# Kernel tuning notes

Hardware: AMD Instinct MI355X
Metric: run time of the kernel (lower is better)

The kernel has to match this reference:

```python
import jax, jax.numpy as jnp
from jax import lax
import numpy as np

WIN_SIZE = 11
WIN_SIGMA = 1.5
K1, K2 = 0.01, 0.03
DATA_RANGE = 1.0


def _gauss_win(size=WIN_SIZE, sigma=WIN_SIGMA):
    coords = np.arange(size, dtype=np.float32) - size // 2
    g = np.exp(-(coords ** 2) / (2.0 * sigma ** 2))
    g /= g.sum()
    return jnp.asarray(g, dtype=jnp.float32)


def _gaussian_blur(x, win):
    # separable depthwise Gaussian blur, VALID padding (as in pytorch-msssim)
    C = x.shape[1]
    dn = ('NCHW', 'OIHW', 'NCHW')
    kh = jnp.tile(win.reshape(1, 1, -1, 1), (C, 1, 1, 1))  # (C,1,K,1)
    kw = jnp.tile(win.reshape(1, 1, 1, -1), (C, 1, 1, 1))  # (C,1,1,K)
    x = lax.conv_general_dilated(x, kh, (1, 1), 'VALID',
                                 dimension_numbers=dn, feature_group_count=C)
    x = lax.conv_general_dilated(x, kw, (1, 1), 'VALID',
                                 dimension_numbers=dn, feature_group_count=C)
    return x


def _ssim_loss(x, y):
    # normalize (-1,1) -> (0,1)
    x = (x + 1.0) * 0.5
    y = (y + 1.0) * 0.5

    c1 = (K1 * DATA_RANGE) ** 2
    c2 = (K2 * DATA_RANGE) ** 2
    win = _gauss_win().astype(x.dtype)

    mu1 = _gaussian_blur(x, win)
    mu2 = _gaussian_blur(y, win)
    mu1_sq = mu1 * mu1
    mu2_sq = mu2 * mu2
    mu1_mu2 = mu1 * mu2

    sigma1_sq = _gaussian_blur(x * x, win) - mu1_sq
    sigma2_sq = _gaussian_blur(y * y, win) - mu2_sq
    sigma12 = _gaussian_blur(x * y, win) - mu1_mu2

    cs_map = (2.0 * sigma12 + c2) / (sigma1_sq + sigma2_sq + c2)
    ssim_map = ((2.0 * mu1_mu2 + c1) / (mu1_sq + mu2_sq + c1)) * cs_map

    # per-channel spatial mean -> nonnegative -> global mean (size_average=True)
    ssim_per_channel = jnp.mean(ssim_map, axis=(2, 3))  # (B, C)
    ssim_per_channel = jax.nn.relu(ssim_per_channel)    # nonnegative_ssim
    return 1.0 - jnp.mean(ssim_per_channel)


def setup_inputs() -> dict:
    key = jax.random.key(0)
    k1, k2 = jax.random.split(key)
    shape = (32, 3, 512, 512)
    return {
        'input': jax.random.normal(k1, shape, dtype=jnp.float32),
        'target': jax.random.normal(k2, shape, dtype=jnp.float32),
    }


def reference(input, target):
    return _ssim_loss(input, target)
```

## Files before the change

### kernel.cpp

```cpp
#include <hip/hip_runtime.h>
#include <math.h>

typedef float f32x2 __attribute__((ext_vector_type(2)));

#define NCH 96
#define HH 512
#define WW 512
#define OH 502
#define STRIP 32
#define NSTRIP 16
#define NT 256

struct Win { float w[11]; };

__device__ __forceinline__ f32x2 pkfma(f32x2 a, f32x2 b, f32x2 c) {
    return __builtin_elementwise_fma(a, b, c);
}

__device__ __forceinline__ float ssim_px(float m1, float m2, float ms, float mp) {
    const float C1v = 1e-4f;
    const float C2v = 9e-4f;
    float mu12  = m1 * m2;
    float musum = fmaf(m1, m1, m2 * m2);
    float num = fmaf(2.f, mp - mu12, C2v) * fmaf(2.f, mu12, C1v);
    float den = ((ms - musum) + C2v) * (musum + C1v);
    return num * __builtin_amdgcn_rcpf(den);
}

#define HB(T0,T1,T2,T3,T4,T5,T6,T7,T8,T9,T10) \
  pkfma(T10, Wv[10], pkfma(T9, Wv[9], pkfma(T8, Wv[8], pkfma(T7, Wv[7], \
  pkfma(T6, Wv[6], pkfma(T5, Wv[5], pkfma(T4, Wv[4], pkfma(T3, Wv[3], \
  pkfma(T2, Wv[2], pkfma(T1, Wv[1], T0 * Wv[0]))))))))))

__global__ __launch_bounds__(NT, 4)
void ssim_main(const float* __restrict__ X, const float* __restrict__ Y,
               float* __restrict__ partial, Win win) {
    __shared__ float4 Eb[2][256];
    __shared__ float4 Ob[2][256];
    __shared__ float red[4];

    const int b     = blockIdx.x;
    const int ch    = b >> 4;
    const int strip = b & 15;
    const int r0    = strip * STRIP;
    const int rows  = min(STRIP, OH - r0);
    const int t     = threadIdx.x;

    f32x2 Wv[11];
    #pragma unroll
    for (int i = 0; i < 11; ++i) Wv[i] = (f32x2){win.w[i], win.w[i]};
    const f32x2 h2 = {0.5f, 0.5f};

    const size_t choff = (size_t)ch * (HH * WW);
    const float* xcol = X + choff + 2 * t;
    const float* ycol = Y + choff + 2 * t;

    f32x2 xs[10], ys[10];

    #pragma unroll
    for (int i = 0; i < 10; ++i) {
        f32x2 xv = *(const f32x2*)(xcol + (size_t)(r0 + i) * WW);
        f32x2 yv = *(const f32x2*)(ycol + (size_t)(r0 + i) * WW);
        xs[i] = pkfma(xv, h2, h2);
        ys[i] = pkfma(yv, h2, h2);
    }
    f32x2 hx = *(const f32x2*)(xcol + (size_t)(r0 + 10) * WW);
    f32x2 hy = *(const f32x2*)(ycol + (size_t)(r0 + 10) * WW);

    float acc = 0.f;

    for (int r = 0; r < rows; ++r) {
        const int buf = r & 1;
        f32x2 nx = pkfma(hx, h2, h2);
        f32x2 ny = pkfma(hy, h2, h2);
        f32x2 ns = pkfma(ny, ny, nx * nx);
        f32x2 np = nx * ny;

        f32x2 vx = nx * Wv[10], vy = ny * Wv[10];
        f32x2 vs = ns * Wv[10], vp = np * Wv[10];
        #pragma unroll
        for (int k = 0; k < 10; ++k) {
            f32x2 xk = xs[k], yk = ys[k];
            f32x2 sk = pkfma(yk, yk, xk * xk);
            f32x2 pk = xk * yk;
            vx = pkfma(xk, Wv[k], vx);
            vy = pkfma(yk, Wv[k], vy);
            vs = pkfma(sk, Wv[k], vs);
            vp = pkfma(pk, Wv[k], vp);
        }
        Eb[buf][t] = make_float4(vx.x, vy.x, vs.x, vp.x);
        Ob[buf][t] = make_float4(vx.y, vy.y, vs.y, vp.y);

        #pragma unroll
        for (int k = 0; k < 9; ++k) { xs[k] = xs[k + 1]; ys[k] = ys[k + 1]; }
        xs[9] = nx; ys[9] = ny;

        {
            const int g = min(r0 + r + 11, HH - 1);
            hx = *(const f32x2*)(xcol + (size_t)g * WW);
            hy = *(const f32x2*)(ycol + (size_t)g * WW);
        }

        __syncthreads();
        if (t <= 250) {
            const float4* Ep = Eb[buf];
            const float4* Op = Ob[buf];
            float4 e0 = Ep[t],     e1 = Ep[t + 1], e2 = Ep[t + 2];
            float4 e3 = Ep[t + 3], e4 = Ep[t + 4], e5 = Ep[t + 5];
            float4 o0 = Op[t],     o1 = Op[t + 1], o2 = Op[t + 2];
            float4 o3 = Op[t + 3], o4 = Op[t + 4], o5 = Op[t + 5];
            f32x2 e0m = {e0.x, e0.y}, e1m = {e1.x, e1.y}, e2m = {e2.x, e2.y};
            f32x2 e3m = {e3.x, e3.y}, e4m = {e4.x, e4.y}, e5m = {e5.x, e5.y};
            f32x2 o0m = {o0.x, o0.y}, o1m = {o1.x, o1.y}, o2m = {o2.x, o2.y};
            f32x2 o3m = {o3.x, o3.y}, o4m = {o4.x, o4.y}, o5m = {o5.x, o5.y};
            f32x2 e0s = {e0.z, e0.w}, e1s = {e1.z, e1.w}, e2s = {e2.z, e2.w};
            f32x2 e3s = {e3.z, e3.w}, e4s = {e4.z, e4.w}, e5s = {e5.z, e5.w};
            f32x2 o0s = {o0.z, o0.w}, o1s = {o1.z, o1.w}, o2s = {o2.z, o2.w};
            f32x2 o3s = {o3.z, o3.w}, o4s = {o4.z, o4.w}, o5s = {o5.z, o5.w};

            f32x2 Am = HB(e0m,o0m,e1m,o1m,e2m,o2m,e3m,o3m,e4m,o4m,e5m);
            f32x2 As = HB(e0s,o0s,e1s,o1s,e2s,o2s,e3s,o3s,e4s,o4s,e5s);
            f32x2 Bm = HB(o0m,e1m,o1m,e2m,o2m,e3m,o3m,e4m,o4m,e5m,o5m);
            f32x2 Bs = HB(o0s,e1s,o1s,e2s,o2s,e3s,o3s,e4s,o4s,e5s,o5s);

            acc += ssim_px(Am.x, Am.y, As.x, As.y);
            acc += ssim_px(Bm.x, Bm.y, Bs.x, Bs.y);
        }
    }

    #pragma unroll
    for (int m = 1; m < 64; m <<= 1) acc += __shfl_xor(acc, m, 64);
    __syncthreads();
    if ((t & 63) == 0) red[t >> 6] = acc;
    __syncthreads();
    if (t == 0) partial[b] = (red[0] + red[1]) + (red[2] + red[3]);
}

__global__ __launch_bounds__(128)
void ssim_final(const float* __restrict__ partial, float* __restrict__ out) {
    const int t = threadIdx.x;
    float v = 0.f;
    if (t < NCH) {
        float s = 0.f;
        #pragma unroll
        for (int i = 0; i < NSTRIP; ++i) s += partial[t * NSTRIP + i];
        s *= (1.f / (502.f * 502.f));
        v = fmaxf(s, 0.f);
    }
    #pragma unroll
    for (int m = 1; m < 64; m <<= 1) v += __shfl_xor(v, m, 64);
    __shared__ float r2[2];
    if ((t & 63) == 0) r2[t >> 6] = v;
    __syncthreads();
    if (t == 0) out[0] = 1.f - (r2[0] + r2[1]) * (1.f / (float)NCH);
}

extern "C" void kernel_launch(void* const* d_in, const int* in_sizes, int n_in,
                              void* d_out, int out_size, void* d_ws, size_t ws_size,
                              hipStream_t stream) {
    const float* X = (const float*)d_in[0];
    const float* Y = (const float*)d_in[1];
    float* out = (float*)d_out;
    float* partial = (float*)d_ws;

    Win win;
    double g[11], sum = 0.0;
    for (int i = 0; i < 11; ++i) {
        double c = (double)(i - 5);
        g[i] = exp(-(c * c) / (2.0 * 1.5 * 1.5));
        sum += g[i];
    }
    for (int i = 0; i < 11; ++i) win.w[i] = (float)(g[i] / sum);

    ssim_main<<<NCH * NSTRIP, NT, 0, stream>>>(X, Y, partial, win);
    ssim_final<<<1, 128, 0, stream>>>(partial, out);
}
```

Before: 86.80 us.

## Compute two output rows per iteration to share vertical-blur work and halve barriers

```diff
diff --git a/kernel.cpp b/kernel.cpp
--- a/kernel.cpp
+++ b/kernel.cpp
@@ -15,6 +15,14 @@
 
 __device__ __forceinline__ f32x2 pkfma(f32x2 a, f32x2 b, f32x2 c) {
     return __builtin_elementwise_fma(a, b, c);
+}
+__device__ __forceinline__ f32x2 pkfmas(f32x2 a, float s, f32x2 c) {
+    f32x2 sv = {s, s};
+    return __builtin_elementwise_fma(a, sv, c);
+}
+__device__ __forceinline__ f32x2 pkmuls(f32x2 a, float s) {
+    f32x2 sv = {s, s};
+    return a * sv;
 }
 
 __device__ __forceinline__ float ssim_px(float m1, float m2, float ms, float mp) {
@@ -28,15 +36,15 @@
 }
 
 #define HB(T0,T1,T2,T3,T4,T5,T6,T7,T8,T9,T10) \
-  pkfma(T10, Wv[10], pkfma(T9, Wv[9], pkfma(T8, Wv[8], pkfma(T7, Wv[7], \
-  pkfma(T6, Wv[6], pkfma(T5, Wv[5], pkfma(T4, Wv[4], pkfma(T3, Wv[3], \
-  pkfma(T2, Wv[2], pkfma(T1, Wv[1], T0 * Wv[0]))))))))))
+  pkfmas(T10, w10, pkfmas(T9, w9, pkfmas(T8, w8, pkfmas(T7, w7, \
+  pkfmas(T6, w6, pkfmas(T5, w5, pkfmas(T4, w4, pkfmas(T3, w3, \
+  pkfmas(T2, w2, pkfmas(T1, w1, pkmuls(T0, w0)))))))))))
 
 __global__ __launch_bounds__(NT, 4)
 void ssim_main(const float* __restrict__ X, const float* __restrict__ Y,
                float* __restrict__ partial, Win win) {
-    __shared__ float4 Eb[2][256];
-    __shared__ float4 Ob[2][256];
+    __shared__ float4 Mb[2][2][256];
+    __shared__ float4 Sb[2][2][256];
     __shared__ float red[4];
 
     const int b     = blockIdx.x;
@@ -46,9 +54,9 @@
     const int rows  = min(STRIP, OH - r0);
     const int t     = threadIdx.x;
 
-    f32x2 Wv[11];
-    #pragma unroll
-    for (int i = 0; i < 11; ++i) Wv[i] = (f32x2){win.w[i], win.w[i]};
+    const float w0 = win.w[0], w1 = win.w[1], w2 = win.w[2], w3 = win.w[3];
+    const float w4 = win.w[4], w5 = win.w[5], w6 = win.w[6], w7 = win.w[7];
+    const float w8 = win.w[8], w9 = win.w[9], w10 = win.w[10];
     const f32x2 h2 = {0.5f, 0.5f};
 
     const size_t choff = (size_t)ch * (HH * WW);
@@ -56,7 +64,6 @@
     const float* ycol = Y + choff + 2 * t;
 
     f32x2 xs[10], ys[10];
-
     #pragma unroll
     for (int i = 0; i < 10; ++i) {
         f32x2 xv = *(const f32x2*)(xcol + (size_t)(r0 + i) * WW);
@@ -64,67 +71,88 @@
         xs[i] = pkfma(xv, h2, h2);
         ys[i] = pkfma(yv, h2, h2);
     }
-    f32x2 hx = *(const f32x2*)(xcol + (size_t)(r0 + 10) * WW);
-    f32x2 hy = *(const f32x2*)(ycol + (size_t)(r0 + 10) * WW);
+    f32x2 hx1 = *(const f32x2*)(xcol + (size_t)(r0 + 10) * WW);
+    f32x2 hy1 = *(const f32x2*)(ycol + (size_t)(r0 + 10) * WW);
+    f32x2 hx2 = *(const f32x2*)(xcol + (size_t)(r0 + 11) * WW);
+    f32x2 hy2 = *(const f32x2*)(ycol + (size_t)(r0 + 11) * WW);
 
     float acc = 0.f;
 
-    for (int r = 0; r < rows; ++r) {
-        const int buf = r & 1;
-        f32x2 nx = pkfma(hx, h2, h2);
-        f32x2 ny = pkfma(hy, h2, h2);
-        f32x2 ns = pkfma(ny, ny, nx * nx);
-        f32x2 np = nx * ny;
-
-        f32x2 vx = nx * Wv[10], vy = ny * Wv[10];
-        f32x2 vs = ns * Wv[10], vp = np * Wv[10];
+    for (int r = 0; r < rows; r += 2) {
+        const int set = (r >> 1) & 1;
+        f32x2 n1x = pkfma(hx1, h2, h2), n1y = pkfma(hy1, h2, h2);
+        f32x2 n2x = pkfma(hx2, h2, h2), n2y = pkfma(hy2, h2, h2);
+        f32x2 n1s = pkfma(n1y, n1y, n1x * n1x), n1p = n1x * n1y;
+        f32x2 n2s = pkfma(n2y, n2y, n2x * n2x), n2p = n2x * n2y;
+
+        f32x2 uAx = pkmuls(n1x, w10), uAy = pkmuls(n1y, w10);
+        f32x2 uAs = pkmuls(n1s, w10), uAp = pkmuls(n1p, w10);
+        f32x2 uBx = pkfmas(n1x, w9, pkmuls(n2x, w10));
+        f32x2 uBy = pkfmas(n1y, w9, pkmuls(n2y, w10));
+        f32x2 uBs = pkfmas(n1s, w9, pkmuls(n2s, w10));
+        f32x2 uBp = pkfmas(n1p, w9, pkmuls(n2p, w10));
         #pragma unroll
         for (int k = 0; k < 10; ++k) {
-            f32x2 xk = xs[k], yk = ys[k];
-            f32x2 sk = pkfma(yk, yk, xk * xk);
-            f32x2 pk = xk * yk;
-            vx = pkfma(xk, Wv[k], vx);
-            vy = pkfma(yk, Wv[k], vy);
-            vs = pkfma(sk, Wv[k], vs);
-            vp = pkfma(pk, Wv[k], vp);
+            const float wk = win.w[k];
+            f32x2 qx = xs[k], qy = ys[k];
+            f32x2 qs = pkfma(qy, qy, qx * qx), qp = qx * qy;
+            uAx = pkfmas(qx, wk, uAx); uAy = pkfmas(qy, wk, uAy);
+            uAs = pkfmas(qs, wk, uAs); uAp = pkfmas(qp, wk, uAp);
+            if (k >= 1) {
+                const float wk1 = win.w[k - 1];
+                uBx = pkfmas(qx, wk1, uBx); uBy = pkfmas(qy, wk1, uBy);
+                uBs = pkfmas(qs, wk1, uBs); uBp = pkfmas(qp, wk1, uBp);
+            }
         }
-        Eb[buf][t] = make_float4(vx.x, vy.x, vs.x, vp.x);
-        Ob[buf][t] = make_float4(vx.y, vy.y, vs.y, vp.y);
+        Mb[set][0][t] = make_float4(uAx.x, uAy.x, uAx.y, uAy.y);
+        Sb[set][0][t] = make_float4(uAs.x, uAp.x, uAs.y, uAp.y);
+        Mb[set][1][t] = make_float4(uBx.x, uBy.x, uBx.y, uBy.y);
+        Sb[set][1][t] = make_float4(uBs.x, uBp.x, uBs.y, uBp.y);
 
         #pragma unroll
-        for (int k = 0; k < 9; ++k) { xs[k] = xs[k + 1]; ys[k] = ys[k + 1]; }
-        xs[9] = nx; ys[9] = ny;
+        for (int k = 0; k < 8; ++k) { xs[k] = xs[k + 2]; ys[k] = ys[k + 2]; }
+        xs[8] = n1x; ys[8] = n1y; xs[9] = n2x; ys[9] = n2y;
 
         {
-            const int g = min(r0 + r + 11, HH - 1);
-            hx = *(const f32x2*)(xcol + (size_t)g * WW);
-            hy = *(const f32x2*)(ycol + (size_t)g * WW);
+            const int g1 = min(r0 + r + 12, HH - 1);
+            const int g2 = min(r0 + r + 13, HH - 1);
+            hx1 = *(const f32x2*)(xcol + (size_t)g1 * WW);
+            hy1 = *(const f32x2*)(ycol + (size_t)g1 * WW);
+            hx2 = *(const f32x2*)(xcol + (size_t)g2 * WW);
+            hy2 = *(const f32x2*)(ycol + (size_t)g2 * WW);
         }
 
         __syncthreads();
         if (t <= 250) {
-            const float4* Ep = Eb[buf];
-            const float4* Op = Ob[buf];
-            float4 e0 = Ep[t],     e1 = Ep[t + 1], e2 = Ep[t + 2];
-            float4 e3 = Ep[t + 3], e4 = Ep[t + 4], e5 = Ep[t + 5];
-            float4 o0 = Op[t],     o1 = Op[t + 1], o2 = Op[t + 2];
-            float4 o3 = Op[t + 3], o4 = Op[t + 4], o5 = Op[t + 5];
-            f32x2 e0m = {e0.x, e0.y}, e1m = {e1.x, e1.y}, e2m = {e2.x, e2.y};
-            f32x2 e3m = {e3.x, e3.y}, e4m = {e4.x, e4.y}, e5m = {e5.x, e5.y};
-            f32x2 o0m = {o0.x, o0.y}, o1m = {o1.x, o1.y}, o2m = {o2.x, o2.y};
-            f32x2 o3m = {o3.x, o3.y}, o4m = {o4.x, o4.y}, o5m = {o5.x, o5.y};
-            f32x2 e0s = {e0.z, e0.w}, e1s = {e1.z, e1.w}, e2s = {e2.z, e2.w};
-            f32x2 e3s = {e3.z, e3.w}, e4s = {e4.z, e4.w}, e5s = {e5.z, e5.w};
-            f32x2 o0s = {o0.z, o0.w}, o1s = {o1.z, o1.w}, o2s = {o2.z, o2.w};
-            f32x2 o3s = {o3.z, o3.w}, o4s = {o4.z, o4.w}, o5s = {o5.z, o5.w};
-
-            f32x2 Am = HB(e0m,o0m,e1m,o1m,e2m,o2m,e3m,o3m,e4m,o4m,e5m);
-            f32x2 As = HB(e0s,o0s,e1s,o1s,e2s,o2s,e3s,o3s,e4s,o4s,e5s);
-            f32x2 Bm = HB(o0m,e1m,o1m,e2m,o2m,e3m,o3m,e4m,o4m,e5m,o5m);
-            f32x2 Bs = HB(o0s,e1s,o1s,e2s,o2s,e3s,o3s,e4s,o4s,e5s,o5s);
-
-            acc += ssim_px(Am.x, Am.y, As.x, As.y);
-            acc += ssim_px(Bm.x, Bm.y, Bs.x, Bs.y);
+            #pragma unroll
+            for (int rr = 0; rr < 2; ++rr) {
+                const float4* Mp = Mb[set][rr];
+                const float4* Sp = Sb[set][rr];
+                float4 m0 = Mp[t],     m1 = Mp[t + 1], m2 = Mp[t + 2];
+                float4 m3 = Mp[t + 3], m4 = Mp[t + 4], m5 = Mp[t + 5];
+                float4 s0 = Sp[t],     s1 = Sp[t + 1], s2 = Sp[t + 2];
+                float4 s3 = Sp[t + 3], s4 = Sp[t + 4], s5 = Sp[t + 5];
+                f32x2 e0m = {m0.x, m0.y}, o0m = {m0.z, m0.w};
+                f32x2 e1m = {m1.x, m1.y}, o1m = {m1.z, m1.w};
+                f32x2 e2m = {m2.x, m2.y}, o2m = {m2.z, m2.w};
+                f32x2 e3m = {m3.x, m3.y}, o3m = {m3.z, m3.w};
+                f32x2 e4m = {m4.x, m4.y}, o4m = {m4.z, m4.w};
+                f32x2 e5m = {m5.x, m5.y}, o5m = {m5.z, m5.w};
+                f32x2 e0s = {s0.x, s0.y}, o0s = {s0.z, s0.w};
+                f32x2 e1s = {s1.x, s1.y}, o1s = {s1.z, s1.w};
+                f32x2 e2s = {s2.x, s2.y}, o2s = {s2.z, s2.w};
+                f32x2 e3s = {s3.x, s3.y}, o3s = {s3.z, s3.w};
+                f32x2 e4s = {s4.x, s4.y}, o4s = {s4.z, s4.w};
+                f32x2 e5s = {s5.x, s5.y}, o5s = {s5.z, s5.w};
+
+                f32x2 Am = HB(e0m,o0m,e1m,o1m,e2m,o2m,e3m,o3m,e4m,o4m,e5m);
+                f32x2 As = HB(e0s,o0s,e1s,o1s,e2s,o2s,e3s,o3s,e4s,o4s,e5s);
+                f32x2 Bm = HB(o0m,e1m,o1m,e2m,o2m,e3m,o3m,e4m,o4m,e5m,o5m);
+                f32x2 Bs = HB(o0s,e1s,o1s,e2s,o2s,e3s,o3s,e4s,o4s,e5s,o5s);
+
+                acc += ssim_px(Am.x, Am.y, As.x, As.y);
+                acc += ssim_px(Bm.x, Bm.y, Bs.x, Bs.y);
+            }
         }
     }
 
```

Result: faster. 78.17 us (-9.9%).
